# Performance work log

Measured on AMD Instinct MI355X. Metric: run time of the kernel, lower is better.

## Reference

```python
import jax, jax.numpy as jnp
import numpy as np

N = 200000   # residue nodes
E = 800000   # backbone edges
P = 500000   # contact pairs to score
DIN = 128    # in_channels['res']
H = 256      # hidden per layer
L = 3        # layers


def _sage(x, src, dst, Wl, Wr, b):
    # SAGEConv: mean-aggregate source-neighbor features into dst, plus root transform
    msum = jax.ops.segment_sum(x[src], dst, num_segments=N)
    deg = jax.ops.segment_sum(jnp.ones((src.shape[0],), x.dtype), dst, num_segments=N)
    m = msum / jnp.maximum(deg, 1.0)[:, None]
    return m @ Wl + x @ Wr + b


def _graphnorm(x, w, b, ms, eps=1e-5):
    # PyG GraphNorm over a single graph (batch of all zeros)
    mu = x.mean(axis=0)
    out = x - ms * mu
    var = (out * out).mean(axis=0)
    return out / jnp.sqrt(var + eps) * w + b


def setup_inputs() -> dict:
    key = jax.random.key(0)
    ks = jax.random.split(key, 40)
    s = 0.05
    inp = {
        'x_res': jax.random.normal(ks[0], (N, DIN), jnp.float32),
        'edge_index': jax.random.randint(ks[1], (2, E), 0, N),
        'contact_pred_index': jax.random.randint(ks[2], (2, P), 0, N),
    }
    dims = [DIN, H, H]
    j = 3
    for i in range(L):
        inp['Wl%d' % i] = jax.random.normal(ks[j], (dims[i], H), jnp.float32) * s; j += 1
        inp['Wr%d' % i] = jax.random.normal(ks[j], (dims[i], H), jnp.float32) * s; j += 1
        inp['bc%d' % i] = jnp.zeros((H,), jnp.float32)
        inp['gnw%d' % i] = jnp.ones((H,), jnp.float32)
        inp['gnb%d' % i] = jnp.zeros((H,), jnp.float32)
        inp['gns%d' % i] = jnp.ones((H,), jnp.float32)
    inp['dyt_alpha'] = jnp.float32(0.5)
    inp['dyt_w'] = jnp.ones((H * L,), jnp.float32)
    inp['dyt_b'] = jnp.zeros((H * L,), jnp.float32)
    XD = [512, 512]
    inp['W1'] = jax.random.normal(ks[j], (H * L, XD[0]), jnp.float32) * s; j += 1
    inp['b1'] = jnp.zeros((XD[0],), jnp.float32)
    inp['W2'] = jax.random.normal(ks[j], (XD[0], XD[1]), jnp.float32) * s; j += 1
    inp['b2'] = jnp.zeros((XD[1],), jnp.float32)
    inp['W3'] = jax.random.normal(ks[j], (XD[1], DIN), jnp.float32) * s; j += 1
    inp['b3'] = jnp.zeros((DIN,), jnp.float32)
    CD = [256, 128]
    inp['C1'] = jax.random.normal(ks[j], (2 * DIN, CD[0]), jnp.float32) * s; j += 1
    inp['c1'] = jnp.zeros((CD[0],), jnp.float32)
    inp['C2'] = jax.random.normal(ks[j], (CD[0], CD[1]), jnp.float32) * s; j += 1
    inp['c2'] = jnp.zeros((CD[1],), jnp.float32)
    inp['C3'] = jax.random.normal(ks[j], (CD[1], 1), jnp.float32) * s; j += 1
    inp['c3'] = jnp.zeros((1,), jnp.float32)
    return inp


def reference(x_res, edge_index, contact_pred_index,
              Wl0, Wr0, bc0, gnw0, gnb0, gns0,
              Wl1, Wr1, bc1, gnw1, gnb1, gns1,
              Wl2, Wr2, bc2, gnw2, gnb2, gns2,
              dyt_alpha, dyt_w, dyt_b,
              W1, b1, W2, b2, W3, b3,
              C1, c1, C2, c2, C3, c3):
    gelu = lambda v: jax.nn.gelu(v, approximate=False)
    src, dst = edge_index[0], edge_index[1]
    inz = x_res
    h = x_res
    layers = [(Wl0, Wr0, bc0, gnw0, gnb0, gns0),
              (Wl1, Wr1, bc1, gnw1, gnb1, gns1),
              (Wl2, Wr2, bc2, gnw2, gnb2, gns2)]
    outs = []
    for i, (Wl, Wr, b, gw, gb, gs) in enumerate(layers):
        prev = h
        h = gelu(_sage(h, src, dst, Wl, Wr, b))
        h = _graphnorm(h, gw, gb, gs)
        if i > 0:
            h = h + prev
        outs.append(h)
    z = jnp.concatenate(outs, axis=1)                 # JumpingKnowledge 'cat' -> [N, 3H]
    z = jnp.tanh(dyt_alpha * z) * dyt_w + dyt_b       # DynamicTanh
    z = gelu(z @ W1 + b1)
    z = gelu(z @ W2 + b2)
    z = z @ W3 + b3
    z = z + inz                                       # residual back to input features
    z = z / (jnp.linalg.norm(z, axis=1, keepdims=True) + 1e-10)
    pair = jnp.concatenate([z[contact_pred_index[0]], z[contact_pred_index[1]]], axis=1)
    e = gelu(pair @ C1 + c1)
    e = gelu(e @ C2 + c2)
    scores = (e @ C3 + c3)[:, 0]
    return jax.nn.sigmoid(scores)
```

## Files before the change

### kernel.cpp

```cpp
#include <hip/hip_runtime.h>
#include <math.h>

typedef unsigned short u16;
typedef __attribute__((ext_vector_type(8))) short short8v;
typedef __attribute__((ext_vector_type(4))) float f32x4;

__device__ __forceinline__ float geluf(float x) {
    return 0.5f * x * (1.0f + erff(x * 0.70710678118654752f));
}
__device__ __forceinline__ float bf2f(u16 u) { return __uint_as_float((unsigned)u << 16); }
__device__ __forceinline__ u16 f2bf(float f) {
    unsigned x = __float_as_uint(f);
    unsigned r = x + 0x7FFFu + ((x >> 16) & 1u);
    return (u16)(r >> 16);
}
__device__ __forceinline__ float tanhfast(float x) {
    float cx = fminf(fmaxf(x, -15.f), 15.f);
    float t = __expf(2.f * cx);
    return (t - 1.f) / (t + 1.f);
}

template<bool BF>
__device__ __forceinline__ float4 ld4(const void* base, long long elemOff) {
    if (BF) {
        ushort4 u = *(const ushort4*)((const u16*)base + elemOff);
        return make_float4(bf2f(u.x), bf2f(u.y), bf2f(u.z), bf2f(u.w));
    } else {
        return *(const float4*)((const float*)base + elemOff);
    }
}

__global__ __launch_bounds__(256) void cnt_kernel(const int* __restrict__ dst, int* __restrict__ cnt, int E, int Nn) {
    int e = blockIdx.x * 256 + threadIdx.x;
    if (e < E) {
        int d = dst[e];
        if ((unsigned)d < (unsigned)Nn) atomicAdd(&cnt[d], 1);
    }
}
__global__ __launch_bounds__(256) void scan1_kernel(const int* __restrict__ cnt, int* __restrict__ rp,
                                                    int* __restrict__ bs, int n) {
    __shared__ int sh[256];
    int i = blockIdx.x * 256 + threadIdx.x;
    int v = (i < n) ? cnt[i] : 0;
    sh[threadIdx.x] = v; __syncthreads();
    for (int o = 1; o < 256; o <<= 1) {
        int t = (threadIdx.x >= o) ? sh[threadIdx.x - o] : 0;
        __syncthreads();
        sh[threadIdx.x] += t;
        __syncthreads();
    }
    if (i < n) rp[i] = sh[threadIdx.x] - v;
    if (threadIdx.x == 255) bs[blockIdx.x] = sh[255];
}
__global__ __launch_bounds__(1024) void scan2_kernel(int* __restrict__ bs, int nb) {
    __shared__ int sh[1024];
    int v = (threadIdx.x < nb) ? bs[threadIdx.x] : 0;
    sh[threadIdx.x] = v; __syncthreads();
    for (int o = 1; o < 1024; o <<= 1) {
        int t = (threadIdx.x >= o) ? sh[threadIdx.x - o] : 0;
        __syncthreads();
        sh[threadIdx.x] += t;
        __syncthreads();
    }
    if (threadIdx.x < nb) bs[threadIdx.x] = sh[threadIdx.x] - v;
}
__global__ __launch_bounds__(256) void scan3_kernel(int* __restrict__ rp, int* __restrict__ cur,
                                                    const int* __restrict__ bs, int n, int E) {
    int i = blockIdx.x * 256 + threadIdx.x;
    if (i < n) {
        int v = rp[i] + bs[blockIdx.x];
        rp[i] = v;
        cur[i] = v;
    }
    if (i == 0) rp[n] = E;
}
__global__ __launch_bounds__(256) void fill_kernel(const int* __restrict__ src, const int* __restrict__ dst,
                                                   int* __restrict__ cur, int* __restrict__ srcs, int E, int Nn) {
    int e = blockIdx.x * 256 + threadIdx.x;
    if (e >= E) return;
    int d = dst[e];
    if ((unsigned)d >= (unsigned)Nn) return;
    int s = src[e];
    if ((unsigned)s >= (unsigned)Nn) s = 0;
    int p = atomicAdd(&cur[d], 1);
    srcs[p] = s;
}

template<bool L0>
__global__ __launch_bounds__(256) void agg_csr_kernel(const void* __restrict__ X, int ldx,
    const int* __restrict__ rp, const int* __restrict__ srcs,
    u16* __restrict__ m, int c0, int rows)
{
    int lrow = blockIdx.x * 4 + (threadIdx.x >> 6);
    if (lrow >= rows) return;
    int lane = threadIdx.x & 63;
    int r = c0 + lrow;
    int b = rp[r], e = rp[r + 1];
    float inv = 1.0f / fmaxf((float)(e - b), 1.0f);
    if (L0) {
        float a0 = 0.f, a1 = 0.f, c0a = 0.f, c1a = 0.f;
        int i = b;
        for (; i + 2 <= e; i += 2) {
            int s0 = srcs[i], s1 = srcs[i + 1];
            float2 v0 = *(const float2*)((const float*)X + (long long)s0 * ldx + lane * 2);
            float2 v1 = *(const float2*)((const float*)X + (long long)s1 * ldx + lane * 2);
            a0 += v0.x; a1 += v0.y;
            c0a += v1.x; c1a += v1.y;
        }
        if (i < e) {
            int s0 = srcs[i];
            float2 v0 = *(const float2*)((const float*)X + (long long)s0 * ldx + lane * 2);
            a0 += v0.x; a1 += v0.y;
        }
        a0 += c0a; a1 += c1a;
        ushort2 o; o.x = f2bf(a0 * inv); o.y = f2bf(a1 * inv);
        *(ushort2*)(m + (long long)lrow * 128 + lane * 2) = o;
    } else {
        float a0 = 0.f, a1 = 0.f, a2 = 0.f, a3 = 0.f;
        float b0 = 0.f, b1 = 0.f, b2 = 0.f, b3 = 0.f;
        int i = b;
        for (; i + 2 <= e; i += 2) {
            int s0 = srcs[i], s1 = srcs[i + 1];
            ushort4 u0 = *(const ushort4*)((const u16*)X + (long long)s0 * ldx + lane * 4);
            ushort4 u1 = *(const ushort4*)((const u16*)X + (long long)s1 * ldx + lane * 4);
            a0 += bf2f(u0.x); a1 += bf2f(u0.y); a2 += bf2f(u0.z); a3 += bf2f(u0.w);
            b0 += bf2f(u1.x); b1 += bf2f(u1.y); b2 += bf2f(u1.z); b3 += bf2f(u1.w);
        }
        if (i < e) {
            int s0 = srcs[i];
            ushort4 u0 = *(const ushort4*)((const u16*)X + (long long)s0 * ldx + lane * 4);
            a0 += bf2f(u0.x); a1 += bf2f(u0.y); a2 += bf2f(u0.z); a3 += bf2f(u0.w);
        }
        a0 += b0; a1 += b1; a2 += b2; a3 += b3;
        ushort4 o;
        o.x = f2bf(a0 * inv); o.y = f2bf(a1 * inv); o.z = f2bf(a2 * inv); o.w = f2bf(a3 * inv);
        *(ushort4*)(m + (long long)lrow * 256 + lane * 4) = o;
    }
}

struct PrepArgs {
    const float* W[11];
    short* outp[11];
    int K[11], Nc[11], kOff[11], Ktot[11];
    int start[12];
};
__global__ __launch_bounds__(256) void prep_all_kernel(PrepArgs a) {
    int idx = blockIdx.x * 256 + threadIdx.x;
    if (idx >= a.start[11]) return;
    int si = 0;
    #pragma unroll
    for (int j = 1; j < 11; ++j) si += (idx >= a.start[j]);
    int local = idx - a.start[si];
    int Nc = a.Nc[si];
    int k = local / Nc, n = local % Nc;
    a.outp[si][(long long)n * a.Ktot[si] + a.kOff[si] + k] = (short)f2bf(a.W[si][local]);
}

template<bool BF>
__device__ __forceinline__ void loadrow(const void* base, long long off, short8v& o0, short8v& o1) {
    if (BF) {
        const short* p = (const short*)base + off;
        o0 = *(const short8v*)p;
        o1 = *(const short8v*)(p + 8);
    } else {
        const float* p = (const float*)base + off;
        float4 a = *(const float4*)p;
        float4 b = *(const float4*)(p + 4);
        float4 c = *(const float4*)(p + 8);
        float4 d = *(const float4*)(p + 12);
        short8v r0, r1;
        r0[0] = (short)f2bf(a.x); r0[1] = (short)f2bf(a.y); r0[2] = (short)f2bf(a.z); r0[3] = (short)f2bf(a.w);
        r0[4] = (short)f2bf(b.x); r0[5] = (short)f2bf(b.y); r0[6] = (short)f2bf(b.z); r0[7] = (short)f2bf(b.w);
        r1[0] = (short)f2bf(c.x); r1[1] = (short)f2bf(c.y); r1[2] = (short)f2bf(c.z); r1[3] = (short)f2bf(c.w);
        r1[4] = (short)f2bf(d.x); r1[5] = (short)f2bf(d.y); r1[6] = (short)f2bf(d.z); r1[7] = (short)f2bf(d.w);
        o0 = r0; o1 = r1;
    }
}

template<int EPI, bool A1BF, bool A2BF, bool CBF, bool STAT, bool NORM>
__global__ __launch_bounds__(256) void mm_kernel(
    const void* __restrict__ A1, int lda1,
    const void* __restrict__ A2, int lda2,
    int K1, int K2,
    const short* __restrict__ Bhi, int ldb,
    const float* __restrict__ bias,
    const float* __restrict__ resid, int ldres,
    float* __restrict__ s1, float* __restrict__ s2,
    void* __restrict__ C, int ldc, int M)
{
    __shared__ short As[128 * 40];
    __shared__ short Bh[128 * 40];
    __shared__ float cst[256];
    __shared__ float rsq[128][2];
    const int t = threadIdx.x;
    const int rowbase = blockIdx.y * 128;
    const int colbase = blockIdx.x * 128;
    const int srow = t >> 1;
    const int sh = (t & 1) << 4;
    const int lane = t & 63;
    const int wv = t >> 6;
    const int wr = (wv >> 1) << 6;
    const int wc = (wv & 1) << 6;
    const int l15 = lane & 15;
    const int kreg = (lane >> 4) << 3;
    const int rgrp = (lane >> 4) << 2;
    if (STAT && t < 256) cst[t] = 0.f;
    f32x4 acc[4][4] = {};
    const int k1t = K1 >> 5;
    const int KT = (K1 + K2) >> 5;

    for (int kt = 0; kt < KT; ++kt) {
        const bool p1 = kt < k1t;
        {
            short8v a0 = {0,0,0,0,0,0,0,0}, a1 = {0,0,0,0,0,0,0,0};
            int r = rowbase + srow;
            if (r < M) {
                const int kbl = (p1 ? kt : kt - k1t) << 5;
                if (p1) loadrow<A1BF>(A1, (long long)r * lda1 + kbl + sh, a0, a1);
                else    loadrow<A2BF>(A2, (long long)r * lda2 + kbl + sh, a0, a1);
            }
            *(short8v*)&As[srow * 40 + sh]     = a0;
            *(short8v*)&As[srow * 40 + sh + 8] = a1;
        }
        {
            long long boff = (long long)(colbase + srow) * ldb + (kt << 5) + sh;
            *(short8v*)&Bh[srow * 40 + sh]     = *(const short8v*)(Bhi + boff);
            *(short8v*)&Bh[srow * 40 + sh + 8] = *(const short8v*)(Bhi + boff + 8);
        }
        __syncthreads();
        short8v a4[4], b4[4];
        #pragma unroll
        for (int mr = 0; mr < 4; ++mr)
            a4[mr] = *(short8v*)&As[(wr + mr * 16 + l15) * 40 + kreg];
        #pragma unroll
        for (int nr = 0; nr < 4; ++nr)
            b4[nr] = *(short8v*)&Bh[(wc + nr * 16 + l15) * 40 + kreg];
        #pragma unroll
        for (int mr = 0; mr < 4; ++mr)
            #pragma unroll
            for (int nr = 0; nr < 4; ++nr)
                acc[mr][nr] = __builtin_amdgcn_mfma_f32_16x16x32_bf16(a4[mr], b4[nr], acc[mr][nr], 0, 0, 0);
        __syncthreads();
    }

    if (NORM) {
        float rs[4][4] = {};
        #pragma unroll
        for (int nr = 0; nr < 4; ++nr) {
            int c = colbase + wc + nr * 16 + l15;
            float bi = bias[c];
            #pragma unroll
            for (int mr = 0; mr < 4; ++mr)
                #pragma unroll
                for (int i = 0; i < 4; ++i) {
                    int r = rowbase + wr + mr * 16 + rgrp + i;
                    float v = 0.f;
                    if (r < M) {
                        v = acc[mr][nr][i] + bi;
                        if (EPI == 3) v += resid[(long long)r * ldres + c];
                        if (EPI == 1) v = geluf(v);
                    }
                    acc[mr][nr][i] = v;
                    rs[mr][i] += v * v;
                }
        }
        #pragma unroll
        for (int mr = 0; mr < 4; ++mr)
            #pragma unroll
            for (int i = 0; i < 4; ++i) {
                float s = rs[mr][i];
                s += __shfl_xor(s, 1); s += __shfl_xor(s, 2);
                s += __shfl_xor(s, 4); s += __shfl_xor(s, 8);
                rs[mr][i] = s;
            }
        if (l15 == 0) {
            #pragma unroll
            for (int mr = 0; mr < 4; ++mr)
                #pragma unroll
                for (int i = 0; i < 4; ++i)
                    rsq[wr + mr * 16 + rgrp + i][wv & 1] = rs[mr][i];
        }
        __syncthreads();
        #pragma unroll
        for (int mr = 0; mr < 4; ++mr)
            #pragma unroll
            for (int i = 0; i < 4; ++i) {
                int rl = wr + mr * 16 + rgrp + i;
                int r = rowbase + rl;
                if (r >= M) continue;
                float inv = 1.0f / (sqrtf(rsq[rl][0] + rsq[rl][1]) + 1e-10f);
                #pragma unroll
                for (int nr = 0; nr < 4; ++nr) {
                    int c = colbase + wc + nr * 16 + l15;
                    float v = acc[mr][nr][i] * inv;
                    if (CBF) ((u16*)C)[(long long)r * ldc + c] = f2bf(v);
                    else     ((float*)C)[(long long)r * ldc + c] = v;
                }
            }
    } else {
        #pragma unroll
        for (int nr = 0; nr < 4; ++nr) {
            int c = colbase + wc + nr * 16 + l15;
            float bi = bias[c];
            float cp = 0.f, cq = 0.f;
            #pragma unroll
            for (int mr = 0; mr < 4; ++mr)
                #pragma unroll
                for (int i = 0; i < 4; ++i) {
                    int r = rowbase + wr + mr * 16 + rgrp + i;
                    if (r >= M) continue;
                    float v = acc[mr][nr][i] + bi;
                    if (EPI == 1) v = geluf(v);
                    if (EPI == 3) v += resid[(long long)r * ldres + c];
                    if (CBF) ((u16*)C)[(long long)r * ldc + c] = f2bf(v);
                    else     ((float*)C)[(long long)r * ldc + c] = v;
                    if (STAT) { cp += v; cq += v * v; }
                }
            if (STAT) {
                cp += __shfl_xor(cp, 16); cp += __shfl_xor(cp, 32);
                cq += __shfl_xor(cq, 16); cq += __shfl_xor(cq, 32);
                if (lane < 16) {
                    int cl = wc + nr * 16 + l15;
                    atomicAdd(&cst[cl], cp);
                    atomicAdd(&cst[128 + cl], cq);
                }
            }
        }
        if (STAT) {
            __syncthreads();
            if (t < 128) {
                atomicAdd(s1 + colbase + t, cst[t]);
                atomicAdd(s2 + colbase + t, cst[128 + t]);
            }
        }
    }
}

__global__ __launch_bounds__(256) void pair_kernel(
    const u16* __restrict__ zf,
    const int* __restrict__ g1, const int* __restrict__ g2,
    int Nn, int P,
    const short* __restrict__ C1t, const float* __restrict__ c1,
    const short* __restrict__ C2t, const float* __restrict__ c2,
    const float* __restrict__ C3, const float* __restrict__ c3,
    float* __restrict__ out)
{
    __shared__ short E1s[64 * 264];
    __shared__ float sc[64][2];
    const int t = threadIdx.x;
    const int lane = t & 63;
    const int wv = t >> 6;
    const int wr = (wv >> 1) << 5;
    const int wc = (wv & 1) << 6;
    const int l15 = lane & 15;
    const int kreg = (lane >> 4) << 3;
    const int rgrp = (lane >> 4) << 2;
    const int p0 = blockIdx.x * 64;

    int gidx[2][2];
    #pragma unroll
    for (int mr = 0; mr < 2; ++mr) {
        int pr = p0 + wr + mr * 16 + l15;
        int a = (pr < P) ? g1[pr] : 0;  if ((unsigned)a >= (unsigned)Nn) a = 0;
        gidx[0][mr] = a;
        int b = (pr < P) ? g2[pr] : 0;  if ((unsigned)b >= (unsigned)Nn) b = 0;
        gidx[1][mr] = b;
    }

    short8v az[2][2][4];
    #pragma unroll
    for (int half = 0; half < 2; ++half)
        #pragma unroll
        for (int mr = 0; mr < 2; ++mr)
            #pragma unroll
            for (int ktl = 0; ktl < 4; ++ktl)
                az[half][mr][ktl] = *(const short8v*)((const short*)zf
                    + (long long)gidx[half][mr] * 128 + (ktl << 5) + kreg);

    #pragma unroll
    for (int ch = 0; ch < 2; ++ch) {
        f32x4 acc1[2][4] = {};
        #pragma unroll
        for (int kt = 0; kt < 8; ++kt) {
            const int half = kt >> 2;
            const int ktl = kt & 3;
            short8v b4[4];
            #pragma unroll
            for (int nr = 0; nr < 4; ++nr)
                b4[nr] = *(const short8v*)(C1t + (long long)(ch * 128 + wc + nr * 16 + l15) * 256 + (kt << 5) + kreg);
            #pragma unroll
            for (int mr = 0; mr < 2; ++mr)
                #pragma unroll
                for (int nr = 0; nr < 4; ++nr)
                    acc1[mr][nr] = __builtin_amdgcn_mfma_f32_16x16x32_bf16(az[half][mr][ktl], b4[nr], acc1[mr][nr], 0, 0, 0);
        }
        #pragma unroll
        for (int nr = 0; nr < 4; ++nr) {
            int cc = wc + nr * 16 + l15;
            float bi = c1[ch * 128 + cc];
            #pragma unroll
            for (int mr = 0; mr < 2; ++mr)
                #pragma unroll
                for (int i = 0; i < 4; ++i) {
                    float v = geluf(acc1[mr][nr][i] + bi);
                    E1s[(wr + mr * 16 + rgrp + i) * 264 + ch * 128 + cc] = (short)f2bf(v);
                }
        }
    }
    __syncthreads();

    f32x4 acc[2][4] = {};
    #pragma unroll
    for (int kt = 0; kt < 8; ++kt) {
        short8v a4[2], b4[4];
        #pragma unroll
        for (int mr = 0; mr < 2; ++mr)
            a4[mr] = *(short8v*)&E1s[(wr + mr * 16 + l15) * 264 + (kt << 5) + kreg];
        #pragma unroll
        for (int nr = 0; nr < 4; ++nr)
            b4[nr] = *(const short8v*)(C2t + (long long)(wc + nr * 16 + l15) * 256 + (kt << 5) + kreg);
        #pragma unroll
        for (int mr = 0; mr < 2; ++mr)
            #pragma unroll
            for (int nr = 0; nr < 4; ++nr)
                acc[mr][nr] = __builtin_amdgcn_mfma_f32_16x16x32_bf16(a4[mr], b4[nr], acc[mr][nr], 0, 0, 0);
    }

    float pr_[2][4] = {};
    #pragma unroll
    for (int nr = 0; nr < 4; ++nr) {
        int cc = wc + nr * 16 + l15;
        float bi = c2[cc];
        float w3 = C3[cc];
        #pragma unroll
        for (int mr = 0; mr < 2; ++mr)
            #pragma unroll
            for (int i = 0; i < 4; ++i)
                pr_[mr][i] += geluf(acc[mr][nr][i] + bi) * w3;
    }
    #pragma unroll
    for (int mr = 0; mr < 2; ++mr)
        #pragma unroll
        for (int i = 0; i < 4; ++i) {
            float s = pr_[mr][i];
            s += __shfl_xor(s, 1); s += __shfl_xor(s, 2);
            s += __shfl_xor(s, 4); s += __shfl_xor(s, 8);
            pr_[mr][i] = s;
        }
    if (l15 == 0) {
        #pragma unroll
        for (int mr = 0; mr < 2; ++mr)
            #pragma unroll
            for (int i = 0; i < 4; ++i)
                sc[wr + mr * 16 + rgrp + i][wv & 1] = pr_[mr][i];
    }
    __syncthreads();
    if (t < 64) {
        int p = p0 + t;
        if (p < P) {
            float x = sc[t][0] + sc[t][1] + c3[0];
            out[p] = 1.0f / (1.0f + expf(-x));
        }
    }
}

template<bool DYT>
__global__ __launch_bounds__(256) void gn_apply_kernel(u16* __restrict__ G, int ldg,
    const u16* __restrict__ prev, int ldp, int M,
    const float* __restrict__ s1, const float* __restrict__ s2,
    const float* __restrict__ gw, const float* __restrict__ gb, const float* __restrict__ gs,
    float invN,
    const float* __restrict__ dA, const float* __restrict__ dW, const float* __restrict__ dB)
{
    long long idx = (long long)blockIdx.x * blockDim.x + threadIdx.x;
    if (idx >= (long long)M * 64) return;
    int c0 = (int)(idx & 63) << 2;
    long long r = idx >> 6;
    float4 g = ld4<true>(G, r * ldg + c0);
    float o[4] = {g.x, g.y, g.z, g.w};
    float alpha = DYT ? dA[0] : 0.f;
    #pragma unroll
    for (int j = 0; j < 4; ++j) {
        int c = c0 + j;
        float mu = s1[c] * invN;
        float ms = gs[c];
        float var = s2[c] * invN - mu * mu * ms * (2.0f - ms);
        float rstd = rsqrtf(var + 1e-5f);
        o[j] = (o[j] - ms * mu) * rstd * gw[c] + gb[c];
    }
    if (prev) {
        float4 pv = ld4<true>(prev, r * ldp + c0);
        o[0] += pv.x; o[1] += pv.y; o[2] += pv.z; o[3] += pv.w;
    }
    if (DYT) {
        #pragma unroll
        for (int j = 0; j < 4; ++j)
            o[j] = tanhfast(alpha * o[j]) * dW[c0 + j] + dB[c0 + j];
    }
    ushort4 u; u.x = f2bf(o[0]); u.y = f2bf(o[1]); u.z = f2bf(o[2]); u.w = f2bf(o[3]);
    *(ushort4*)((u16*)G + r * ldg + c0) = u;
}

__global__ __launch_bounds__(256) void dyt512_kernel(u16* __restrict__ Z,
    const float* __restrict__ alphaP, const float* __restrict__ w, const float* __restrict__ b,
    long long total)
{
    long long idx = (long long)blockIdx.x * blockDim.x + threadIdx.x;
    if (idx >= total) return;
    int c0 = (int)(idx & 63) << 3;
    long long r = idx >> 6;
    float alpha = alphaP[0];
    short8v z = *(short8v*)(Z + r * 768 + c0);
    float4 w0 = *(const float4*)(w + c0);
    float4 w1 = *(const float4*)(w + c0 + 4);
    float4 b0 = *(const float4*)(b + c0);
    float4 b1 = *(const float4*)(b + c0 + 4);
    short8v o;
    o[0] = (short)f2bf(tanhfast(alpha * bf2f((u16)z[0])) * w0.x + b0.x);
    o[1] = (short)f2bf(tanhfast(alpha * bf2f((u16)z[1])) * w0.y + b0.y);
    o[2] = (short)f2bf(tanhfast(alpha * bf2f((u16)z[2])) * w0.z + b0.z);
    o[3] = (short)f2bf(tanhfast(alpha * bf2f((u16)z[3])) * w0.w + b0.w);
    o[4] = (short)f2bf(tanhfast(alpha * bf2f((u16)z[4])) * w1.x + b1.x);
    o[5] = (short)f2bf(tanhfast(alpha * bf2f((u16)z[5])) * w1.y + b1.y);
    o[6] = (short)f2bf(tanhfast(alpha * bf2f((u16)z[6])) * w1.z + b1.z);
    o[7] = (short)f2bf(tanhfast(alpha * bf2f((u16)z[7])) * w1.w + b1.w);
    *(short8v*)(Z + r * 768 + c0) = o;
}

extern "C" void kernel_launch(void* const* d_in, const int* in_sizes, int n_in,
                              void* d_out, int out_size, void* d_ws, size_t ws_size,
                              hipStream_t stream) {
    const float* x_res = (const float*)d_in[0];
    const int* eidx = (const int*)d_in[1];
    const int* cidx = (const int*)d_in[2];
    const int N = in_sizes[0] / 128;
    const int E = in_sizes[1] / 2;
    const int P = in_sizes[2] / 2;
    const int* src = eidx;
    const int* dst = eidx + E;
    const int* g1 = cidx;
    const int* g2 = cidx + P;
    const float* Wl[3] = {(const float*)d_in[3], (const float*)d_in[9],  (const float*)d_in[15]};
    const float* Wr[3] = {(const float*)d_in[4], (const float*)d_in[10], (const float*)d_in[16]};
    const float* bc[3] = {(const float*)d_in[5], (const float*)d_in[11], (const float*)d_in[17]};
    const float* gnw[3] = {(const float*)d_in[6], (const float*)d_in[12], (const float*)d_in[18]};
    const float* gnb[3] = {(const float*)d_in[7], (const float*)d_in[13], (const float*)d_in[19]};
    const float* gns[3] = {(const float*)d_in[8], (const float*)d_in[14], (const float*)d_in[20]};
    const float* alphaP = (const float*)d_in[21];
    const float* dytw = (const float*)d_in[22];
    const float* dytb = (const float*)d_in[23];
    const float* W1 = (const float*)d_in[24]; const float* b1 = (const float*)d_in[25];
    const float* W2 = (const float*)d_in[26]; const float* b2 = (const float*)d_in[27];
    const float* W3 = (const float*)d_in[28]; const float* b3 = (const float*)d_in[29];
    const float* C1 = (const float*)d_in[30]; const float* c1 = (const float*)d_in[31];
    const float* C2 = (const float*)d_in[32]; const float* c2 = (const float*)d_in[33];
    const float* C3 = (const float*)d_in[34]; const float* c3 = (const float*)d_in[35];
    float* out = (float*)d_out;

    char* ws = (char*)d_ws;
    size_t off = 0;
    size_t zOff  = off; off += (size_t)N * 768 * 2;     off = (off + 255) & ~(size_t)255;
    size_t stOff = off; off += 4096;                    off = (off + 255) & ~(size_t)255;
    size_t zfOff = off; off += (size_t)N * 128 * 2;     off = (off + 255) & ~(size_t)255;
    size_t rpOff = off; off += (size_t)(N + 1) * 4;     off = (off + 255) & ~(size_t)255;
    size_t curOff = off; off += (size_t)N * 4;          off = (off + 255) & ~(size_t)255;
    size_t srcsOff = off; off += (size_t)E * 4;         off = (off + 255) & ~(size_t)255;
    size_t bsOff = off; off += 4096;                    off = (off + 255) & ~(size_t)255;
    static const size_t se[8] = {65536, 131072, 131072, 393216, 262144, 65536, 65536, 32768};
    short* wt[8];
    for (int i = 0; i < 8; ++i) {
        wt[i] = (short*)(ws + off);
        off += 2 * se[i];
        off = (off + 255) & ~(size_t)255;
    }
    size_t pOff = off;
    size_t avail = ws_size > pOff ? ws_size - pOff : 0;

    u16*   Z    = (u16*)(ws + zOff);
    float* st   = (float*)(ws + stOff);
    u16*   zf   = (u16*)(ws + zfOff);
    int*   rp   = (int*)(ws + rpOff);
    int*   cur  = (int*)(ws + curOff);
    int*   srcs = (int*)(ws + srcsOff);
    int*   bs   = (int*)(ws + bsOff);
    u16*   pbuf = (u16*)(ws + pOff);

    int NC = (int)((avail /  512) & ~(size_t)127); if (NC < 128) NC = 128; if (NC > N) NC = N;
    int S  = (int)((avail / 2048) & ~(size_t)127); if (S  < 128) S  = 128; if (S  > N) S  = N;

    dim3 blk(256);

    {
        PrepArgs a;
        const float* Ws[11] = {Wl[0], Wr[0], Wl[1], Wr[1], Wl[2], Wr[2], W1, W2, W3, C1, C2};
        short* Os[11] = {wt[0], wt[0], wt[1], wt[1], wt[2], wt[2], wt[3], wt[4], wt[5], wt[6], wt[7]};
        int Ks[11]    = {128, 128, 256, 256, 256, 256, 768, 512, 512, 256, 256};
        int Ncs[11]   = {256, 256, 256, 256, 256, 256, 512, 512, 128, 256, 128};
        int kOffs[11] = {0, 128, 0, 256, 0, 256, 0, 0, 0, 0, 0};
        int Ktots[11] = {256, 256, 512, 512, 512, 512, 768, 512, 512, 256, 256};
        int s = 0;
        for (int i = 0; i < 11; ++i) {
            a.W[i] = Ws[i]; a.outp[i] = Os[i];
            a.K[i] = Ks[i]; a.Nc[i] = Ncs[i]; a.kOff[i] = kOffs[i]; a.Ktot[i] = Ktots[i];
            a.start[i] = s;
            s += Ks[i] * Ncs[i];
        }
        a.start[11] = s;
        prep_all_kernel<<<(s + 255) / 256, 256, 0, stream>>>(a);
    }

    int nb = (N + 255) / 256;
    hipMemsetAsync(cur, 0, (size_t)N * 4, stream);
    cnt_kernel<<<(E + 255) / 256, 256, 0, stream>>>(dst, cur, E, N);
    scan1_kernel<<<nb, 256, 0, stream>>>(cur, rp, bs, N);
    scan2_kernel<<<1, 1024, 0, stream>>>(bs, nb);
    scan3_kernel<<<nb, 256, 0, stream>>>(rp, cur, bs, N, E);
    fill_kernel<<<(E + 255) / 256, 256, 0, stream>>>(src, dst, cur, srcs, E, N);

    u16* m = pbuf;
    for (int l = 0; l < 3; ++l) {
        u16* Zl = Z + l * 256;
        hipMemsetAsync(st, 0, 512 * 4, stream);
        for (int c0 = 0; c0 < N; c0 += NC) {
            int rows = (N - c0 < NC) ? (N - c0) : NC;
            int aggblocks = (rows + 3) / 4;
            dim3 grid(2, (rows + 127) / 128);
            if (l == 0) {
                agg_csr_kernel<true><<<aggblocks, 256, 0, stream>>>(x_res, 128, rp, srcs, m, c0, rows);
                mm_kernel<1, true, false, true, true, false><<<grid, blk, 0, stream>>>(
                    m, 128, x_res + (size_t)c0 * 128, 128, 128, 128,
                    wt[0], 256, bc[0], nullptr, 0, st, st + 256,
                    Zl + (size_t)c0 * 768, 768, rows);
            } else {
                const u16* h = Z + (l - 1) * 256;
                agg_csr_kernel<false><<<aggblocks, 256, 0, stream>>>(h, 768, rp, srcs, m, c0, rows);
                mm_kernel<1, true, true, true, true, false><<<grid, blk, 0, stream>>>(
                    m, 256, h + (size_t)c0 * 768, 768, 256, 256,
                    wt[l], 512, bc[l], nullptr, 0, st, st + 256,
                    Zl + (size_t)c0 * 768, 768, rows);
            }
        }
        const u16* prev = (l == 0) ? nullptr : (Z + (l - 1) * 256);
        int gnblocks = (int)(((long long)N * 64 + 255) / 256);
        if (l == 2)
            gn_apply_kernel<true><<<gnblocks, 256, 0, stream>>>(
                Zl, 768, prev, 768, N, st, st + 256, gnw[l], gnb[l], gns[l], 1.0f / (float)N,
                alphaP, dytw + 512, dytb + 512);
        else
            gn_apply_kernel<false><<<gnblocks, 256, 0, stream>>>(
                Zl, 768, prev, 768, N, st, st + 256, gnw[l], gnb[l], gns[l], 1.0f / (float)N,
                nullptr, nullptr, nullptr);
    }

    dyt512_kernel<<<(int)(((long long)N * 64 + 255) / 256), 256, 0, stream>>>(
        Z, alphaP, dytw, dytb, (long long)N * 64);

    {
        short* t1c = (short*)pbuf;
        short* t2c = t1c + (size_t)S * 512;
        for (int r0 = 0; r0 < N; r0 += S) {
            int rows = (N - r0 < S) ? (N - r0) : S;
            mm_kernel<1, true, true, true, false, false><<<dim3(4, (rows + 127) / 128), blk, 0, stream>>>(
                Z + (size_t)r0 * 768, 768, nullptr, 0, 768, 0,
                wt[3], 768, b1, nullptr, 0, nullptr, nullptr, t1c, 512, rows);
            mm_kernel<1, true, true, true, false, false><<<dim3(4, (rows + 127) / 128), blk, 0, stream>>>(
                t1c, 512, nullptr, 0, 512, 0,
                wt[4], 512, b2, nullptr, 0, nullptr, nullptr, t2c, 512, rows);
            mm_kernel<3, true, true, true, false, true><<<dim3(1, (rows + 127) / 128), blk, 0, stream>>>(
                t2c, 512, nullptr, 0, 512, 0,
                wt[5], 512, b3, x_res + (size_t)r0 * 128, 128, nullptr, nullptr,
                zf + (size_t)r0 * 128, 128, rows);
        }
    }

    pair_kernel<<<(P + 63) / 64, blk, 0, stream>>>(
        zf, g1, g2, N, P, wt[6], c1, wt[7], c2, C3, c3, out);
}
```

Baseline: 3.263 ms.

## Bucket-sort contact pairs by first node index to improve gather locality

Result: slower. 3.476 ms (+6.5%).

```diff
diff --git a/kernel.cpp b/kernel.cpp
--- a/kernel.cpp
+++ b/kernel.cpp
@@ -84,6 +84,26 @@
     if ((unsigned)s >= (unsigned)Nn) s = 0;
     int p = atomicAdd(&cur[d], 1);
     srcs[p] = s;
+}
+
+__global__ __launch_bounds__(256) void pcnt_kernel(const int* __restrict__ g1, int* __restrict__ bcnt,
+                                                   int P, int Nn) {
+    int p = blockIdx.x * 256 + threadIdx.x;
+    if (p >= P) return;
+    int g = g1[p];
+    if ((unsigned)g >= (unsigned)Nn) g = 0;
+    int b = (int)(((long long)g << 10) / Nn);
+    atomicAdd(&bcnt[b], 1);
+}
+__global__ __launch_bounds__(256) void pfill_kernel(const int* __restrict__ g1, int* __restrict__ bcur,
+                                                    int* __restrict__ perm, int P, int Nn) {
+    int p = blockIdx.x * 256 + threadIdx.x;
+    if (p >= P) return;
+    int g = g1[p];
+    if ((unsigned)g >= (unsigned)Nn) g = 0;
+    int b = (int)(((long long)g << 10) / Nn);
+    int pos = atomicAdd(&bcur[b], 1);
+    perm[pos] = p;
 }
 
 template<bool L0>
@@ -339,6 +359,7 @@
 __global__ __launch_bounds__(256) void pair_kernel(
     const u16* __restrict__ zf,
     const int* __restrict__ g1, const int* __restrict__ g2,
+    const int* __restrict__ perm,
     int Nn, int P,
     const short* __restrict__ C1t, const float* __restrict__ c1,
     const short* __restrict__ C2t, const float* __restrict__ c2,
@@ -361,9 +382,10 @@
     #pragma unroll
     for (int mr = 0; mr < 2; ++mr) {
         int pr = p0 + wr + mr * 16 + l15;
-        int a = (pr < P) ? g1[pr] : 0;  if ((unsigned)a >= (unsigned)Nn) a = 0;
+        int pp = (pr < P) ? perm[pr] : 0;
+        int a = g1[pp];  if ((unsigned)a >= (unsigned)Nn) a = 0;
         gidx[0][mr] = a;
-        int b = (pr < P) ? g2[pr] : 0;  if ((unsigned)b >= (unsigned)Nn) b = 0;
+        int b = g2[pp];  if ((unsigned)b >= (unsigned)Nn) b = 0;
         gidx[1][mr] = b;
     }
 
@@ -459,7 +481,7 @@
         int p = p0 + t;
         if (p < P) {
             float x = sc[t][0] + sc[t][1] + c3[0];
-            out[p] = 1.0f / (1.0f + expf(-x));
+            out[perm[p]] = 1.0f / (1.0f + expf(-x));
         }
     }
 }
@@ -566,6 +588,7 @@
     size_t curOff = off; off += (size_t)N * 4;          off = (off + 255) & ~(size_t)255;
     size_t srcsOff = off; off += (size_t)E * 4;         off = (off + 255) & ~(size_t)255;
     size_t bsOff = off; off += 4096;                    off = (off + 255) & ~(size_t)255;
+    size_t permOff = off; off += (size_t)P * 4;         off = (off + 255) & ~(size_t)255;
     static const size_t se[8] = {65536, 131072, 131072, 393216, 262144, 65536, 65536, 32768};
     short* wt[8];
     for (int i = 0; i < 8; ++i) {
@@ -583,6 +606,7 @@
     int*   cur  = (int*)(ws + curOff);
     int*   srcs = (int*)(ws + srcsOff);
     int*   bs   = (int*)(ws + bsOff);
+    int*   perm = (int*)(ws + permOff);
     u16*   pbuf = (u16*)(ws + pOff);
 
     int NC = (int)((avail /  512) & ~(size_t)127); if (NC < 128) NC = 128; if (NC > N) NC = N;
@@ -616,6 +640,11 @@
     scan2_kernel<<<1, 1024, 0, stream>>>(bs, nb);
     scan3_kernel<<<nb, 256, 0, stream>>>(rp, cur, bs, N, E);
     fill_kernel<<<(E + 255) / 256, 256, 0, stream>>>(src, dst, cur, srcs, E, N);
+
+    hipMemsetAsync(bs, 0, 4096, stream);
+    pcnt_kernel<<<(P + 255) / 256, 256, 0, stream>>>(g1, bs, P, N);
+    scan2_kernel<<<1, 1024, 0, stream>>>(bs, 1024);
+    pfill_kernel<<<(P + 255) / 256, 256, 0, stream>>>(g1, bs, perm, P, N);
 
     u16* m = pbuf;
     for (int l = 0; l < 3; ++l) {
@@ -674,5 +703,5 @@
     }
 
     pair_kernel<<<(P + 63) / 64, blk, 0, stream>>>(
-        zf, g1, g2, N, P, wt[6], c1, wt[7], c2, C3, c3, out);
-}
+        zf, g1, g2, perm, N, P, wt[6], c1, wt[7], c2, C3, c3, out);
+}
```
